# Kernel optimization log

Hardware: AMD Instinct MI355X
Metric: run time of the kernel (lower is better)

Reference implementation:

```python
import jax, jax.numpy as jnp
import numpy as np

EMB_DIM = 1024
D_K = 64
B, S = 4, 4096

def setup_inputs() -> dict:
    key = jax.random.key(0)
    ks = jax.random.split(key, 8)
    inv = 1.0 / np.sqrt(EMB_DIM)
    return {
        "input1": jax.random.normal(ks[0], (B, S, EMB_DIM), dtype=jnp.float32),
        "input2": jax.random.normal(ks[1], (B, S, EMB_DIM), dtype=jnp.float32),
        "Wq": jax.random.uniform(ks[2], (EMB_DIM, D_K), jnp.float32, -inv, inv),
        "bq": jax.random.uniform(ks[3], (D_K,), jnp.float32, -inv, inv),
        "Wk": jax.random.uniform(ks[4], (EMB_DIM, D_K), jnp.float32, -inv, inv),
        "bk": jax.random.uniform(ks[5], (D_K,), jnp.float32, -inv, inv),
        "Wv": jax.random.uniform(ks[6], (EMB_DIM, D_K), jnp.float32, -inv, inv),
        "bv": jax.random.uniform(ks[7], (D_K,), jnp.float32, -inv, inv),
    }

def reference(input1, input2, Wq, bq, Wk, bk, Wv, bv):
    # queries from input2; keys/values from input1 (as in the torch forward)
    q = input2 @ Wq + bq            # [B, Sq, d_k]
    k = input1 @ Wk + bk            # [B, Sk, d_k]
    v = input1 @ Wv + bv            # [B, Sk, d_k]
    scale = 1.0 / jnp.sqrt(jnp.asarray(D_K, q.dtype))
    scores = jnp.einsum("bqd,bkd->bqk", q, k) * scale  # [B, Sq, Sk]
    attn = jax.nn.softmax(scores, axis=-1)
    return jnp.einsum("bqk,bkd->bqd", attn, v)          # [B, Sq, d_k]
```

## Files before the change

kernel.cpp:

```cpp
#include <hip/hip_runtime.h>
#include <hip/hip_bf16.h>

#define E 1024
#define DK 64
#define SEQ 4096
#define NB 4
#define KSCALE 0.18033688011112042f

typedef short bf16x8 __attribute__((ext_vector_type(8)));
typedef short bf16x4 __attribute__((ext_vector_type(4)));
typedef float f32x4 __attribute__((ext_vector_type(4)));

typedef const __attribute__((address_space(1))) unsigned int* gcp;
typedef __attribute__((address_space(3))) unsigned int* lcp;

__device__ inline unsigned short f2bf(float f) {
    unsigned int u = __float_as_uint(f);
    u += 0x7fff + ((u >> 16) & 1);
    return (unsigned short)(u >> 16);
}
__device__ inline unsigned int cvtpk(float a, float b) {
    union { __hip_bfloat162 h; unsigned int u; } x;
    x.h = __float22bfloat162_rn(make_float2(a, b));
    return x.u;
}
__device__ inline bf16x8 cvt8(f32x4 a, f32x4 b) {
    union { unsigned int u[4]; bf16x8 v; } x;
    x.u[0] = cvtpk(a[0], a[1]); x.u[1] = cvtpk(a[2], a[3]);
    x.u[2] = cvtpk(b[0], b[1]); x.u[3] = cvtpk(b[2], b[3]);
    return x.v;
}

__global__ __launch_bounds__(256) void wt_kernel(
    const float* __restrict__ Wq, const float* __restrict__ Wk, const float* __restrict__ Wv,
    unsigned short* __restrict__ wtq, unsigned short* __restrict__ wtk, unsigned short* __restrict__ wtv)
{
    const float* src; unsigned short* dst;
    if (blockIdx.y == 0)      { src = Wq; dst = wtq; }
    else if (blockIdx.y == 1) { src = Wk; dst = wtk; }
    else                      { src = Wv; dst = wtv; }
    const int tid = threadIdx.x;
    const int e0 = blockIdx.x * 64;
    __shared__ float Ws[64][65];
    #pragma unroll
    for (int i = 0; i < 4; ++i) {
        int flat = i * 256 + tid;
        int r = flat >> 4;
        int c4 = (flat & 15) << 2;
        float4 v = *reinterpret_cast<const float4*>(&src[(size_t)(e0 + r) * DK + c4]);
        Ws[c4 + 0][r] = v.x; Ws[c4 + 1][r] = v.y; Ws[c4 + 2][r] = v.z; Ws[c4 + 3][r] = v.w;
    }
    __syncthreads();
    #pragma unroll
    for (int i = 0; i < 4; ++i) {
        int flat = i * 256 + tid;
        int c = flat >> 4;
        int r4 = (flat & 15) << 2;
        ushort4 o;
        o.x = f2bf(Ws[c][r4 + 0]); o.y = f2bf(Ws[c][r4 + 1]);
        o.z = f2bf(Ws[c][r4 + 2]); o.w = f2bf(Ws[c][r4 + 3]);
        *reinterpret_cast<ushort4*>(&dst[(size_t)c * E + e0 + r4]) = o;
    }
}

__global__ __launch_bounds__(256, 4) void proj_kernel(
    const float* __restrict__ in_q, const float* __restrict__ in_kv,
    const unsigned short* __restrict__ wtq, const unsigned short* __restrict__ wtk,
    const unsigned short* __restrict__ wtv,
    const float* __restrict__ bq, const float* __restrict__ bk, const float* __restrict__ bv,
    unsigned short* __restrict__ Qw, unsigned short* __restrict__ Kw, unsigned short* __restrict__ Vtw)
{
    const int tid = threadIdx.x;
    const int w = tid >> 6, lane = tid & 63, quad = lane >> 4, l16 = lane & 15;
    const int row0 = blockIdx.x * 64;
    const bool isQ = (blockIdx.y == 0);
    const float* Arow = (isQ ? in_q : in_kv) + (size_t)(row0 + w * 16 + l16) * E;
    const unsigned short* w0 = isQ ? wtq : wtk;

    __shared__ unsigned short W0s[2][4096];
    __shared__ unsigned short W1s[2][4096];

    const int rl = lane >> 3, pp = lane & 7;

    #pragma unroll
    for (int i = 0; i < 2; ++i) {
        int g = w * 2 + i;
        int r = g * 8 + rl;
        int lc = pp ^ (r & 7);
        __builtin_amdgcn_global_load_lds((gcp)(const void*)(w0 + (size_t)r * E + lc * 8),
                                         (lcp)(void*)&W0s[0][g * 512], 16, 0, 0);
        if (!isQ)
            __builtin_amdgcn_global_load_lds((gcp)(const void*)(wtv + (size_t)r * E + lc * 8),
                                             (lcp)(void*)&W1s[0][g * 512], 16, 0, 0);
    }
    f32x4 a_cur[4];
    #pragma unroll
    for (int ks = 0; ks < 2; ++ks)
        #pragma unroll
        for (int j = 0; j < 2; ++j)
            a_cur[ks * 2 + j] = *reinterpret_cast<const f32x4*>(Arow + ks * 32 + quad * 8 + j * 4);
    __syncthreads();

    f32x4 acc0[4] = {};
    f32x4 acc1[4] = {};

    for (int kb = 0; kb < 16; ++kb) {
        const int cur = kb & 1, nxt = cur ^ 1;
        f32x4 a_nxt[4];
        if (kb < 15) {
            const int ko = (kb + 1) * 64;
            #pragma unroll
            for (int i = 0; i < 2; ++i) {
                int g = w * 2 + i;
                int r = g * 8 + rl;
                int lc = pp ^ (r & 7);
                __builtin_amdgcn_global_load_lds((gcp)(const void*)(w0 + (size_t)r * E + ko + lc * 8),
                                                 (lcp)(void*)&W0s[nxt][g * 512], 16, 0, 0);
                if (!isQ)
                    __builtin_amdgcn_global_load_lds((gcp)(const void*)(wtv + (size_t)r * E + ko + lc * 8),
                                                     (lcp)(void*)&W1s[nxt][g * 512], 16, 0, 0);
            }
            const float* an = Arow + ko;
            #pragma unroll
            for (int ks = 0; ks < 2; ++ks)
                #pragma unroll
                for (int j = 0; j < 2; ++j)
                    a_nxt[ks * 2 + j] = *reinterpret_cast<const f32x4*>(an + ks * 32 + quad * 8 + j * 4);
        }
        #pragma unroll
        for (int ks = 0; ks < 2; ++ks) {
            bf16x8 af = cvt8(a_cur[ks * 2], a_cur[ks * 2 + 1]);
            #pragma unroll
            for (int ct = 0; ct < 4; ++ct) {
                int brow = ct * 16 + l16;
                int pc = (ks * 4 + quad) ^ (brow & 7);
                bf16x8 b0 = *reinterpret_cast<const bf16x8*>(&W0s[cur][brow * 64 + pc * 8]);
                acc0[ct] = __builtin_amdgcn_mfma_f32_16x16x32_bf16(af, b0, acc0[ct], 0, 0, 0);
                if (!isQ) {
                    bf16x8 b1 = *reinterpret_cast<const bf16x8*>(&W1s[cur][brow * 64 + pc * 8]);
                    acc1[ct] = __builtin_amdgcn_mfma_f32_16x16x32_bf16(af, b1, acc1[ct], 0, 0, 0);
                }
            }
        }
        #pragma unroll
        for (int j = 0; j < 4; ++j) a_cur[j] = a_nxt[j];
        if (kb < 15) __syncthreads();
    }

    const int orow0 = row0 + w * 16 + quad * 4;
    #pragma unroll
    for (int ct = 0; ct < 4; ++ct) {
        int col = ct * 16 + l16;
        if (isQ) {
            float bias = bq[col];
            #pragma unroll
            for (int r = 0; r < 4; ++r)
                Qw[(size_t)(orow0 + r) * DK + col] = f2bf(acc0[ct][r] + bias);
        } else {
            float biask = bk[col], biasv = bv[col];
            #pragma unroll
            for (int r = 0; r < 4; ++r) {
                int grow = orow0 + r;
                Kw[(size_t)grow * DK + col] = f2bf((acc0[ct][r] + biask) * KSCALE);
                int bb = grow >> 12;
                int tok = grow & 4095;
                Vtw[((size_t)(bb * 64 + col)) * SEQ + tok] = f2bf(acc1[ct][r] + biasv);
            }
        }
    }
}

__global__ __launch_bounds__(512) void attn_kernel(
    const unsigned short* __restrict__ Qw, const unsigned short* __restrict__ Kw,
    const unsigned short* __restrict__ Vtw, float* __restrict__ out)
{
    const int tid = threadIdx.x;
    const int w = tid >> 6, lane = tid & 63, quad = lane >> 4, l16 = lane & 15;
    const int wk = w & 3, wp = w >> 2;
    const int b = (blockIdx.x & 7) >> 1;
    const int qt = ((blockIdx.x >> 3) << 1) | (blockIdx.x & 1);

    __shared__ unsigned short Klds[2][8192];
    __shared__ unsigned short Vlds[2][8192];
    __shared__ float LDSf[8][2][16][68];
    __shared__ float LDSl[8][4][16];

    const unsigned short* Ksrc = Kw + (size_t)b * SEQ * DK;
    const unsigned short* Vsrc = Vtw + (size_t)b * 64 * SEQ;

    const int g0 = w * 2, g1 = w * 2 + 1;
    const int krow0 = g0 * 8 + (lane >> 3), krow1 = g1 * 8 + (lane >> 3);
    const int kcol = ((lane & 7) ^ (lane >> 3)) << 4;
    const int vrow0 = g0 * 4 + (lane >> 4), vrow1 = g1 * 4 + (lane >> 4);
    const int vcol0 = ((lane & 15) ^ (vrow0 & 7)) << 4;
    const int vcol1 = ((lane & 15) ^ (vrow1 & 7)) << 4;

    auto stage = [&](int t, int bb) {
        const char* kb = (const char*)Ksrc + (size_t)t * 16384;
        __builtin_amdgcn_global_load_lds((gcp)(const void*)(kb + krow0 * 128 + kcol),
                                         (lcp)(void*)((char*)Klds[bb] + g0 * 1024), 16, 0, 0);
        __builtin_amdgcn_global_load_lds((gcp)(const void*)(kb + krow1 * 128 + kcol),
                                         (lcp)(void*)((char*)Klds[bb] + g1 * 1024), 16, 0, 0);
        const char* vb = (const char*)Vsrc + t * 256;
        __builtin_amdgcn_global_load_lds((gcp)(const void*)(vb + (size_t)vrow0 * 8192 + vcol0),
                                         (lcp)(void*)((char*)Vlds[bb] + g0 * 1024), 16, 0, 0);
        __builtin_amdgcn_global_load_lds((gcp)(const void*)(vb + (size_t)vrow1 * 8192 + vcol1),
                                         (lcp)(void*)((char*)Vlds[bb] + g1 * 1024), 16, 0, 0);
    };

    stage(0, 0);

    bf16x8 qfb[2][4];
    #pragma unroll
    for (int ks = 0; ks < 2; ++ks)
        #pragma unroll
        for (int ct = 0; ct < 4; ++ct)
            qfb[ks][ct] = *reinterpret_cast<const bf16x8*>(
                &Qw[((size_t)(b * SEQ + qt * 64 + ct * 16 + l16)) * DK + ks * 32 + quad * 8]);

    const int kxor = (l16 & 7) << 4;
    const int krow = wp * 64 + wk * 16 + l16;
    const unsigned kf0_off = (unsigned)(krow * 128 + ((quad * 16) ^ kxor));
    const unsigned kf1_off = (unsigned)(krow * 128 + ((64 + quad * 16) ^ kxor));
    unsigned va_off[4];
    #pragma unroll
    for (int ct = 0; ct < 4; ++ct)
        va_off[ct] = (unsigned)((ct * 16 + l16) * 256 +
                                ((wp * 128 + wk * 32 + quad * 8) ^ kxor));

    __syncthreads();

    float lp[4] = {0.f, 0.f, 0.f, 0.f};
    f32x4 o[4][4] = {};

    #pragma unroll 2
    for (int i = 0; i < 32; ++i) {
        const int cur = i & 1;
        if (i < 31) stage(i + 1, cur ^ 1);

        bf16x8 kf0 = *reinterpret_cast<const bf16x8*>((const char*)Klds[cur] + kf0_off);
        bf16x8 kf1 = *reinterpret_cast<const bf16x8*>((const char*)Klds[cur] + kf1_off);
        bf16x4 va[4];
        #pragma unroll
        for (int ct = 0; ct < 4; ++ct)
            va[ct] = *reinterpret_cast<const bf16x4*>((const char*)Vlds[cur] + va_off[ct]);

        f32x4 sacc[4] = {};
        #pragma unroll
        for (int ct = 0; ct < 4; ++ct) {
            sacc[ct] = __builtin_amdgcn_mfma_f32_16x16x32_bf16(kf0, qfb[0][ct], sacc[ct], 0, 0, 0);
            sacc[ct] = __builtin_amdgcn_mfma_f32_16x16x32_bf16(kf1, qfb[1][ct], sacc[ct], 0, 0, 0);
        }

        #pragma unroll
        for (int cq = 0; cq < 4; ++cq) {
            float p0 = __builtin_amdgcn_exp2f(sacc[cq][0]);
            float p1 = __builtin_amdgcn_exp2f(sacc[cq][1]);
            float p2 = __builtin_amdgcn_exp2f(sacc[cq][2]);
            float p3 = __builtin_amdgcn_exp2f(sacc[cq][3]);
            lp[cq] += (p0 + p1) + (p2 + p3);
            union { unsigned int u[2]; bf16x4 v; } pbu;
            pbu.u[0] = cvtpk(p0, p1);
            pbu.u[1] = cvtpk(p2, p3);
            bf16x4 pb = pbu.v;
            #pragma unroll
            for (int cd = 0; cd < 4; ++cd)
                o[cd][cq] = __builtin_amdgcn_mfma_f32_16x16x16bf16_1k(va[cd], pb, o[cd][cq], 0, 0, 0);
        }

        __syncthreads();
    }

    #pragma unroll
    for (int cq = 0; cq < 4; ++cq) {
        float t = lp[cq];
        t += __shfl_xor(t, 16, 64);
        t += __shfl_xor(t, 32, 64);
        lp[cq] = t;
    }
    if (lane < 16)
        #pragma unroll
        for (int cq = 0; cq < 4; ++cq)
            LDSl[w][cq][lane] = lp[cq];

    #pragma unroll
    for (int rr = 0; rr < 2; ++rr) {
        #pragma unroll
        for (int hh = 0; hh < 2; ++hh)
            #pragma unroll
            for (int cd = 0; cd < 4; ++cd)
                *reinterpret_cast<f32x4*>(&LDSf[w][hh][l16][cd * 16 + quad * 4]) = o[cd][rr * 2 + hh];
        __syncthreads();
        {
            const int hh = tid >> 8;
            const int cq = rr * 2 + hh;
            const int ql = (tid >> 4) & 15;
            const int d4 = (tid & 15) << 2;
            f32x4 acc = {};
            #pragma unroll
            for (int w2 = 0; w2 < 8; ++w2)
                acc += *reinterpret_cast<const f32x4*>(&LDSf[w2][hh][ql][d4]);
            float lq = 0.f;
            #pragma unroll
            for (int w2 = 0; w2 < 8; ++w2)
                lq += LDSl[w2][cq][ql];
            f32x4 res = acc * (1.0f / lq);
            *reinterpret_cast<f32x4*>(&out[((size_t)(b * SEQ + qt * 64 + cq * 16 + ql)) * DK + d4]) = res;
        }
        __syncthreads();
    }
}

extern "C" void kernel_launch(void* const* d_in, const int* in_sizes, int n_in,
                              void* d_out, int out_size, void* d_ws, size_t ws_size,
                              hipStream_t stream) {
    const float* input1 = (const float*)d_in[0];
    const float* input2 = (const float*)d_in[1];
    const float* Wq = (const float*)d_in[2];
    const float* bq = (const float*)d_in[3];
    const float* Wk = (const float*)d_in[4];
    const float* bk = (const float*)d_in[5];
    const float* Wv = (const float*)d_in[6];
    const float* bv = (const float*)d_in[7];
    float* out = (float*)d_out;

    char* ws = (char*)d_ws;
    unsigned short* wtq = (unsigned short*)(ws + 0);
    unsigned short* wtk = (unsigned short*)(ws + 131072);
    unsigned short* wtv = (unsigned short*)(ws + 262144);
    unsigned short* Qw  = (unsigned short*)(ws + 393216);
    unsigned short* Kw  = (unsigned short*)(ws + 2490368);
    unsigned short* Vtw = (unsigned short*)(ws + 4587520);

    wt_kernel<<<dim3(16, 3), 256, 0, stream>>>(Wq, Wk, Wv, wtq, wtk, wtv);
    proj_kernel<<<dim3(256, 2), 256, 0, stream>>>(input2, input1, wtq, wtk, wtv,
                                                  bq, bk, bv, Qw, Kw, Vtw);
    attn_kernel<<<dim3(256), 512, 0, stream>>>(Qw, Kw, Vtw, out);
}
```

Baseline: 209.6 us.

## Stage projection A tiles via async LDS loads and coalesce output stores

The projection kernel now streams the fp32 input rows into a swizzled, double-buffered LDS buffer with global_load_lds, replacing the per-thread register prefetch with strided row reads. The epilogue writes results into an LDS tile (transposed for V) and then emits 16-byte vectorized, coalesced stores for Q, K and Vt, replacing scattered 2-byte stores, especially the strided Vt transpose writes. This adds 32KB of LDS per block, which may cut occupancy under launch_bounds(256,4), and adds an unconditional barrier on every iteration.

```diff
diff --git a/kernel.cpp b/kernel.cpp
--- a/kernel.cpp
+++ b/kernel.cpp
@@ -10,6 +10,7 @@
 typedef short bf16x8 __attribute__((ext_vector_type(8)));
 typedef short bf16x4 __attribute__((ext_vector_type(4)));
 typedef float f32x4 __attribute__((ext_vector_type(4)));
+typedef unsigned short u16x8 __attribute__((ext_vector_type(8)));
 
 typedef const __attribute__((address_space(1))) unsigned int* gcp;
 typedef __attribute__((address_space(3))) unsigned int* lcp;
@@ -74,13 +75,27 @@
     const int w = tid >> 6, lane = tid & 63, quad = lane >> 4, l16 = lane & 15;
     const int row0 = blockIdx.x * 64;
     const bool isQ = (blockIdx.y == 0);
-    const float* Arow = (isQ ? in_q : in_kv) + (size_t)(row0 + w * 16 + l16) * E;
+    const float* A0 = isQ ? in_q : in_kv;
     const unsigned short* w0 = isQ ? wtq : wtk;
 
     __shared__ unsigned short W0s[2][4096];
     __shared__ unsigned short W1s[2][4096];
+    __shared__ char ABuf[32768];
 
     const int rl = lane >> 3, pp = lane & 7;
+
+    const int ar = (w * 4) * 4 + (lane >> 4);
+    auto stageA = [&](int kb, int bb) {
+        #pragma unroll
+        for (int i = 0; i < 4; ++i) {
+            int g = w * 4 + i;
+            int r = ar + i * 4;
+            int cc = (lane & 15) ^ (r & 15);
+            __builtin_amdgcn_global_load_lds(
+                (gcp)(const void*)(A0 + (size_t)(row0 + r) * E + kb * 64 + cc * 4),
+                (lcp)(void*)(ABuf + bb * 16384 + g * 1024), 16, 0, 0);
+        }
+    };
 
     #pragma unroll
     for (int i = 0; i < 2; ++i) {
@@ -93,20 +108,17 @@
             __builtin_amdgcn_global_load_lds((gcp)(const void*)(wtv + (size_t)r * E + lc * 8),
                                              (lcp)(void*)&W1s[0][g * 512], 16, 0, 0);
     }
-    f32x4 a_cur[4];
-    #pragma unroll
-    for (int ks = 0; ks < 2; ++ks)
-        #pragma unroll
-        for (int j = 0; j < 2; ++j)
-            a_cur[ks * 2 + j] = *reinterpret_cast<const f32x4*>(Arow + ks * 32 + quad * 8 + j * 4);
+    stageA(0, 0);
     __syncthreads();
 
     f32x4 acc0[4] = {};
     f32x4 acc1[4] = {};
 
+    const int arow = w * 16 + l16;
+    const char* Arow_lds = ABuf + arow * 256;
+
     for (int kb = 0; kb < 16; ++kb) {
         const int cur = kb & 1, nxt = cur ^ 1;
-        f32x4 a_nxt[4];
         if (kb < 15) {
             const int ko = (kb + 1) * 64;
             #pragma unroll
@@ -120,16 +132,15 @@
                     __builtin_amdgcn_global_load_lds((gcp)(const void*)(wtv + (size_t)r * E + ko + lc * 8),
                                                      (lcp)(void*)&W1s[nxt][g * 512], 16, 0, 0);
             }
-            const float* an = Arow + ko;
-            #pragma unroll
-            for (int ks = 0; ks < 2; ++ks)
-                #pragma unroll
-                for (int j = 0; j < 2; ++j)
-                    a_nxt[ks * 2 + j] = *reinterpret_cast<const f32x4*>(an + ks * 32 + quad * 8 + j * 4);
+            stageA(kb + 1, nxt);
         }
         #pragma unroll
         for (int ks = 0; ks < 2; ++ks) {
-            bf16x8 af = cvt8(a_cur[ks * 2], a_cur[ks * 2 + 1]);
+            f32x4 a0 = *reinterpret_cast<const f32x4*>(
+                Arow_lds + cur * 16384 + ((ks * 8 + quad * 2 + 0) ^ l16) * 16);
+            f32x4 a1 = *reinterpret_cast<const f32x4*>(
+                Arow_lds + cur * 16384 + ((ks * 8 + quad * 2 + 1) ^ l16) * 16);
+            bf16x8 af = cvt8(a0, a1);
             #pragma unroll
             for (int ct = 0; ct < 4; ++ct) {
                 int brow = ct * 16 + l16;
@@ -142,12 +153,12 @@
                 }
             }
         }
-        #pragma unroll
-        for (int j = 0; j < 4; ++j) a_cur[j] = a_nxt[j];
-        if (kb < 15) __syncthreads();
-    }
-
-    const int orow0 = row0 + w * 16 + quad * 4;
+        __syncthreads();
+    }
+
+    unsigned short (*Cs0)[72] = reinterpret_cast<unsigned short(*)[72]>(ABuf);
+    unsigned short (*Cs1)[72] = reinterpret_cast<unsigned short(*)[72]>(ABuf + 9216);
+    const int tl0 = w * 16 + quad * 4;
     #pragma unroll
     for (int ct = 0; ct < 4; ++ct) {
         int col = ct * 16 + l16;
@@ -155,17 +166,30 @@
             float bias = bq[col];
             #pragma unroll
             for (int r = 0; r < 4; ++r)
-                Qw[(size_t)(orow0 + r) * DK + col] = f2bf(acc0[ct][r] + bias);
+                Cs0[tl0 + r][col] = f2bf(acc0[ct][r] + bias);
         } else {
             float biask = bk[col], biasv = bv[col];
             #pragma unroll
             for (int r = 0; r < 4; ++r) {
-                int grow = orow0 + r;
-                Kw[(size_t)grow * DK + col] = f2bf((acc0[ct][r] + biask) * KSCALE);
-                int bb = grow >> 12;
-                int tok = grow & 4095;
-                Vtw[((size_t)(bb * 64 + col)) * SEQ + tok] = f2bf(acc1[ct][r] + biasv);
+                Cs0[tl0 + r][col] = f2bf((acc0[ct][r] + biask) * KSCALE);
+                Cs1[col][tl0 + r] = f2bf(acc1[ct][r] + biasv);
             }
+        }
+    }
+    __syncthreads();
+
+    const int bb = row0 >> 12, tok0 = row0 & 4095;
+    #pragma unroll
+    for (int jj = 0; jj < 2; ++jj) {
+        int rr = w * 16 + jj * 8 + (lane >> 3);
+        int c8 = (lane & 7) * 8;
+        u16x8 v0 = *reinterpret_cast<const u16x8*>(&Cs0[rr][c8]);
+        if (isQ) {
+            *reinterpret_cast<u16x8*>(&Qw[(size_t)(row0 + rr) * DK + c8]) = v0;
+        } else {
+            *reinterpret_cast<u16x8*>(&Kw[(size_t)(row0 + rr) * DK + c8]) = v0;
+            u16x8 v1 = *reinterpret_cast<const u16x8*>(&Cs1[rr][c8]);
+            *reinterpret_cast<u16x8*>(&Vtw[((size_t)(bb * 64 + rr)) * SEQ + tok0 + c8]) = v1;
         }
     }
 }
```

Measured after the change: 210.9 us. Within noise of the previous version (+0.6%).

## Split attention over key halves with per-warp query groups and combine kernel

Applied to the files above, without the earlier changes.

Each attention block now handles 128 queries over half of the keys: the two warp groups take different 64-query sets instead of splitting the keys, and each warp does two 16-key subtiles per staged 128-key tile. Partial unnormalized outputs and row sums go to workspace, and a new combine kernel adds the two halves and normalizes. This doubles the reuse of each staged K/V tile across queries and halves the loop trip count. The cost is extra global traffic for the partial results plus one more kernel launch.

```diff
diff --git a/kernel.cpp b/kernel.cpp
--- a/kernel.cpp
+++ b/kernel.cpp
@@ -172,21 +172,22 @@
 
 __global__ __launch_bounds__(512) void attn_kernel(
     const unsigned short* __restrict__ Qw, const unsigned short* __restrict__ Kw,
-    const unsigned short* __restrict__ Vtw, float* __restrict__ out)
+    const unsigned short* __restrict__ Vtw, float* __restrict__ Opart, float* __restrict__ Lpart)
 {
     const int tid = threadIdx.x;
     const int w = tid >> 6, lane = tid & 63, quad = lane >> 4, l16 = lane & 15;
-    const int wk = w & 3, wp = w >> 2;
-    const int b = (blockIdx.x & 7) >> 1;
-    const int qt = ((blockIdx.x >> 3) << 1) | (blockIdx.x & 1);
+    const int s = w & 3, h = w >> 2;
+    const int kh = blockIdx.x & 1;
+    const int b  = (blockIdx.x >> 1) & 3;
+    const int qt = blockIdx.x >> 3;
 
     __shared__ unsigned short Klds[2][8192];
     __shared__ unsigned short Vlds[2][8192];
     __shared__ float LDSf[8][2][16][68];
     __shared__ float LDSl[8][4][16];
 
-    const unsigned short* Ksrc = Kw + (size_t)b * SEQ * DK;
-    const unsigned short* Vsrc = Vtw + (size_t)b * 64 * SEQ;
+    const unsigned short* Ksrc = Kw + ((size_t)b * SEQ + kh * 2048) * DK;
+    const unsigned short* Vsrc = Vtw + (size_t)b * 64 * SEQ + kh * 2048;
 
     const int g0 = w * 2, g1 = w * 2 + 1;
     const int krow0 = g0 * 8 + (lane >> 3), krow1 = g1 * 8 + (lane >> 3);
@@ -216,56 +217,63 @@
         #pragma unroll
         for (int ct = 0; ct < 4; ++ct)
             qfb[ks][ct] = *reinterpret_cast<const bf16x8*>(
-                &Qw[((size_t)(b * SEQ + qt * 64 + ct * 16 + l16)) * DK + ks * 32 + quad * 8]);
+                &Qw[((size_t)(b * SEQ + qt * 128 + h * 64 + ct * 16 + l16)) * DK + ks * 32 + quad * 8]);
 
     const int kxor = (l16 & 7) << 4;
-    const int krow = wp * 64 + wk * 16 + l16;
-    const unsigned kf0_off = (unsigned)(krow * 128 + ((quad * 16) ^ kxor));
-    const unsigned kf1_off = (unsigned)(krow * 128 + ((64 + quad * 16) ^ kxor));
-    unsigned va_off[4];
-    #pragma unroll
-    for (int ct = 0; ct < 4; ++ct)
-        va_off[ct] = (unsigned)((ct * 16 + l16) * 256 +
-                                ((wp * 128 + wk * 32 + quad * 8) ^ kxor));
+    unsigned kf_off[2][2];
+    unsigned va_off[2][4];
+    #pragma unroll
+    for (int t2 = 0; t2 < 2; ++t2) {
+        const int kr = s * 32 + t2 * 16 + l16;
+        kf_off[t2][0] = (unsigned)(kr * 128 + ((quad * 16) ^ kxor));
+        kf_off[t2][1] = (unsigned)(kr * 128 + ((64 + quad * 16) ^ kxor));
+        #pragma unroll
+        for (int ct = 0; ct < 4; ++ct)
+            va_off[t2][ct] = (unsigned)((ct * 16 + l16) * 256 +
+                                        ((s * 64 + t2 * 32 + quad * 8) ^ kxor));
+    }
 
     __syncthreads();
 
     float lp[4] = {0.f, 0.f, 0.f, 0.f};
     f32x4 o[4][4] = {};
 
-    #pragma unroll 2
-    for (int i = 0; i < 32; ++i) {
+    #pragma unroll 1
+    for (int i = 0; i < 16; ++i) {
         const int cur = i & 1;
-        if (i < 31) stage(i + 1, cur ^ 1);
-
-        bf16x8 kf0 = *reinterpret_cast<const bf16x8*>((const char*)Klds[cur] + kf0_off);
-        bf16x8 kf1 = *reinterpret_cast<const bf16x8*>((const char*)Klds[cur] + kf1_off);
-        bf16x4 va[4];
-        #pragma unroll
-        for (int ct = 0; ct < 4; ++ct)
-            va[ct] = *reinterpret_cast<const bf16x4*>((const char*)Vlds[cur] + va_off[ct]);
-
-        f32x4 sacc[4] = {};
-        #pragma unroll
-        for (int ct = 0; ct < 4; ++ct) {
-            sacc[ct] = __builtin_amdgcn_mfma_f32_16x16x32_bf16(kf0, qfb[0][ct], sacc[ct], 0, 0, 0);
-            sacc[ct] = __builtin_amdgcn_mfma_f32_16x16x32_bf16(kf1, qfb[1][ct], sacc[ct], 0, 0, 0);
-        }
-
-        #pragma unroll
-        for (int cq = 0; cq < 4; ++cq) {
-            float p0 = __builtin_amdgcn_exp2f(sacc[cq][0]);
-            float p1 = __builtin_amdgcn_exp2f(sacc[cq][1]);
-            float p2 = __builtin_amdgcn_exp2f(sacc[cq][2]);
-            float p3 = __builtin_amdgcn_exp2f(sacc[cq][3]);
-            lp[cq] += (p0 + p1) + (p2 + p3);
-            union { unsigned int u[2]; bf16x4 v; } pbu;
-            pbu.u[0] = cvtpk(p0, p1);
-            pbu.u[1] = cvtpk(p2, p3);
-            bf16x4 pb = pbu.v;
-            #pragma unroll
-            for (int cd = 0; cd < 4; ++cd)
-                o[cd][cq] = __builtin_amdgcn_mfma_f32_16x16x16bf16_1k(va[cd], pb, o[cd][cq], 0, 0, 0);
+        if (i < 15) stage(i + 1, cur ^ 1);
+
+        #pragma unroll
+        for (int t2 = 0; t2 < 2; ++t2) {
+            bf16x8 kf0 = *reinterpret_cast<const bf16x8*>((const char*)Klds[cur] + kf_off[t2][0]);
+            bf16x8 kf1 = *reinterpret_cast<const bf16x8*>((const char*)Klds[cur] + kf_off[t2][1]);
+            bf16x4 va[4];
+            #pragma unroll
+            for (int ct = 0; ct < 4; ++ct)
+                va[ct] = *reinterpret_cast<const bf16x4*>((const char*)Vlds[cur] + va_off[t2][ct]);
+
+            f32x4 sacc[4] = {};
+            #pragma unroll
+            for (int ct = 0; ct < 4; ++ct) {
+                sacc[ct] = __builtin_amdgcn_mfma_f32_16x16x32_bf16(kf0, qfb[0][ct], sacc[ct], 0, 0, 0);
+                sacc[ct] = __builtin_amdgcn_mfma_f32_16x16x32_bf16(kf1, qfb[1][ct], sacc[ct], 0, 0, 0);
+            }
+
+            #pragma unroll
+            for (int cq = 0; cq < 4; ++cq) {
+                float p0 = __builtin_amdgcn_exp2f(sacc[cq][0]);
+                float p1 = __builtin_amdgcn_exp2f(sacc[cq][1]);
+                float p2 = __builtin_amdgcn_exp2f(sacc[cq][2]);
+                float p3 = __builtin_amdgcn_exp2f(sacc[cq][3]);
+                lp[cq] += (p0 + p1) + (p2 + p3);
+                union { unsigned int u[2]; bf16x4 v; } pbu;
+                pbu.u[0] = cvtpk(p0, p1);
+                pbu.u[1] = cvtpk(p2, p3);
+                bf16x4 pb = pbu.v;
+                #pragma unroll
+                for (int cd = 0; cd < 4; ++cd)
+                    o[cd][cq] = __builtin_amdgcn_mfma_f32_16x16x16bf16_1k(va[cd], pb, o[cd][cq], 0, 0, 0);
+            }
         }
 
         __syncthreads();
@@ -283,6 +291,7 @@
         for (int cq = 0; cq < 4; ++cq)
             LDSl[w][cq][lane] = lp[cq];
 
+    const int rowbase = b * SEQ + qt * 128;
     #pragma unroll
     for (int rr = 0; rr < 2; ++rr) {
         #pragma unroll
@@ -291,23 +300,44 @@
             for (int cd = 0; cd < 4; ++cd)
                 *reinterpret_cast<f32x4*>(&LDSf[w][hh][l16][cd * 16 + quad * 4]) = o[cd][rr * 2 + hh];
         __syncthreads();
-        {
-            const int hh = tid >> 8;
-            const int cq = rr * 2 + hh;
-            const int ql = (tid >> 4) & 15;
-            const int d4 = (tid & 15) << 2;
+        #pragma unroll
+        for (int p = 0; p < 2; ++p) {
+            const int item = tid + p * 512;
+            const int h2 = item >> 9, rem = item & 511;
+            const int j = rem >> 8, ql = (rem >> 4) & 15, d4 = (rem & 15) << 2;
+            const int cq = rr * 2 + j;
             f32x4 acc = {};
             #pragma unroll
-            for (int w2 = 0; w2 < 8; ++w2)
-                acc += *reinterpret_cast<const f32x4*>(&LDSf[w2][hh][ql][d4]);
-            float lq = 0.f;
-            #pragma unroll
-            for (int w2 = 0; w2 < 8; ++w2)
-                lq += LDSl[w2][cq][ql];
-            f32x4 res = acc * (1.0f / lq);
-            *reinterpret_cast<f32x4*>(&out[((size_t)(b * SEQ + qt * 64 + cq * 16 + ql)) * DK + d4]) = res;
+            for (int w2 = 0; w2 < 4; ++w2)
+                acc += *reinterpret_cast<const f32x4*>(&LDSf[h2 * 4 + w2][j][ql][d4]);
+            const int row = rowbase + h2 * 64 + cq * 16 + ql;
+            *reinterpret_cast<f32x4*>(&Opart[((size_t)kh * (NB * SEQ) + row) * DK + d4]) = acc;
+            if ((rem & 15) == 0) {
+                float lq = 0.f;
+                #pragma unroll
+                for (int w2 = 0; w2 < 4; ++w2)
+                    lq += LDSl[h2 * 4 + w2][cq][ql];
+                Lpart[kh * (NB * SEQ) + row] = lq;
+            }
         }
         __syncthreads();
+    }
+}
+
+__global__ __launch_bounds__(256) void comb_kernel(
+    const float* __restrict__ Op, const float* __restrict__ Lp, float* __restrict__ out)
+{
+    const int idx = blockIdx.x * 256 + threadIdx.x;
+    #pragma unroll
+    for (int it = 0; it < 4; ++it) {
+        const int c = idx + it * 65536;
+        const int row = c >> 4;
+        const int d4 = (c & 15) << 2;
+        f32x4 a = *reinterpret_cast<const f32x4*>(&Op[(size_t)row * DK + d4]);
+        f32x4 b2 = *reinterpret_cast<const f32x4*>(&Op[(size_t)(NB * SEQ + row) * DK + d4]);
+        float l = Lp[row] + Lp[NB * SEQ + row];
+        f32x4 r = (a + b2) * (1.0f / l);
+        *reinterpret_cast<f32x4*>(&out[(size_t)row * DK + d4]) = r;
     }
 }
 
@@ -331,9 +361,12 @@
     unsigned short* Qw  = (unsigned short*)(ws + 393216);
     unsigned short* Kw  = (unsigned short*)(ws + 2490368);
     unsigned short* Vtw = (unsigned short*)(ws + 4587520);
+    float* Opart = (float*)(ws + 6684672);
+    float* Lpart = (float*)(ws + 15073280);
 
     wt_kernel<<<dim3(16, 3), 256, 0, stream>>>(Wq, Wk, Wv, wtq, wtk, wtv);
     proj_kernel<<<dim3(256, 2), 256, 0, stream>>>(input2, input1, wtq, wtk, wtv,
                                                   bq, bk, bv, Qw, Kw, Vtw);
-    attn_kernel<<<dim3(256), 512, 0, stream>>>(Qw, Kw, Vtw, out);
-}
+    attn_kernel<<<dim3(256), 512, 0, stream>>>(Qw, Kw, Vtw, Opart, Lpart);
+    comb_kernel<<<dim3(256), 256, 0, stream>>>(Opart, Lpart, out);
+}
```

Measured after the change: 197.2 us. 5.9% less time.
